# Kernel optimization log

Measured on AMD Instinct MI355X. Metric: run time of the kernel, lower is better.

The kernel has to match this reference:

```python
import jax, jax.numpy as jnp
import numpy as np

N_HEADS = 16


def setup_inputs() -> dict:
    key = jax.random.key(0)
    k_x, k_q, k_k, k_v, k_o = jax.random.split(key, 5)
    N, S, D = 8, 4096, 1024
    scale = 0.02
    return {
        "x": jax.random.normal(k_x, (N, S, D), dtype=jnp.float32),
        "Wq": jax.random.normal(k_q, (D, D), dtype=jnp.float32) * scale,
        "Wk": jax.random.normal(k_k, (D, D), dtype=jnp.float32) * scale,
        "Wv": jax.random.normal(k_v, (D, D), dtype=jnp.float32) * scale,
        "Wo": jax.random.normal(k_o, (D, D), dtype=jnp.float32) * scale,
        "bo": jnp.zeros((D,), dtype=jnp.float32),
    }


def reference(x, Wq, Wk, Wv, Wo, bo):
    N, S, D = x.shape
    H = N_HEADS
    hd = D // H
    # torch nn.Linear: y = x @ W.T (no bias for q/k/v)
    q = (x @ Wq.T).reshape(N, S, H, hd).transpose(0, 2, 1, 3)  # (N, H, S, hd)
    k = (x @ Wk.T).reshape(N, S, H, hd).transpose(0, 2, 1, 3)
    v = (x @ Wv.T).reshape(N, S, H, hd).transpose(0, 2, 1, 3)
    # Faithful to source: labels q/k bind to the HEADS axis of the permuted
    # tensors, h binds to the sequence axis -> attention over heads, shape
    # (N, S, H, H).
    att = jnp.einsum('nqhd,nkhd->nhqk', q, k)
    att = jax.nn.softmax(att / jnp.sqrt(jnp.asarray(hd, x.dtype)), axis=3)
    out = jnp.einsum('nhqk,nkhd->nqhd', att, v).reshape(N, S, D)
    return out @ Wo.T + bo
```

## Files before the change

kernel.cpp:

```cpp
#include <hip/hip_runtime.h>
#include <hip/hip_bf16.h>
#include <stdint.h>

typedef __hip_bfloat16 bf16;
typedef __attribute__((ext_vector_type(8))) short short8;
typedef __attribute__((ext_vector_type(4))) float f32x4;

__device__ __forceinline__ unsigned short f2bf(float f) {
    bf16 h = __float2bfloat16(f);
    union { bf16 h; unsigned short u; } c; c.h = h; return c.u;
}
__device__ __forceinline__ unsigned int pack2(float a, float b) {
    return (unsigned int)f2bf(a) | ((unsigned int)f2bf(b) << 16);
}

__device__ __forceinline__ void gld16(const void* g, void* l) {
    __builtin_amdgcn_global_load_lds(
        (const __attribute__((address_space(1))) void*)g,
        (__attribute__((address_space(3))) void*)l, 16, 0, 0);
}

__global__ __launch_bounds__(256) void cvt_f32_bf16(
    const float* __restrict__ in, unsigned short* __restrict__ out, long n4)
{
    long i = (long)blockIdx.x * 256 + threadIdx.x;
    if (i >= n4) return;
    float4 v = ((const float4*)in)[i];
    ushort4 o;
    o.x = f2bf(v.x); o.y = f2bf(v.y); o.z = f2bf(v.z); o.w = f2bf(v.w);
    ((ushort4*)out)[i] = o;
}

__global__ __launch_bounds__(256) void cvt_w4(
    const float* __restrict__ a, const float* __restrict__ b,
    const float* __restrict__ c, const float* __restrict__ d,
    unsigned short* __restrict__ out)
{
    const float* src = (blockIdx.y == 0) ? a : (blockIdx.y == 1) ? b
                     : (blockIdx.y == 2) ? c : d;
    long i = (long)blockIdx.x * 256 + threadIdx.x;
    float4 v = ((const float4*)src)[i];
    ushort4 o;
    o.x = f2bf(v.x); o.y = f2bf(v.y); o.z = f2bf(v.z); o.w = f2bf(v.w);
    ((ushort4*)(out + (size_t)blockIdx.y * 1048576))[i] = o;
}

#define BM 128
#define BN 128
#define BK 32

__device__ __forceinline__ void store_c(bf16* C, size_t idx, float v) {
    C[idx] = __float2bfloat16(v);
}
__device__ __forceinline__ void store_c(float* C, size_t idx, float v) {
    C[idx] = v;
}

template <typename CT>
__device__ __forceinline__ void gemm_body(
    const bf16* __restrict__ A, const bf16* __restrict__ B,
    CT* __restrict__ C, const float* __restrict__ bias,
    int M, int N, int K)
{
    __shared__ char smem[(BM * BK + BN * BK) * 2];
    char* sA = smem;
    char* sB = smem + BM * BK * 2;

    const int t    = threadIdx.x;
    const int lane = t & 63;
    const int wave = t >> 6;
    const int wm   = wave & 1;
    const int wn   = wave >> 1;
    const int l16  = lane & 15;
    const int quad = lane >> 4;

    const int rowBase = blockIdx.y * BM;
    const int colBase = blockIdx.x * BN;

    f32x4 acc[4][4];
#pragma unroll
    for (int i = 0; i < 4; i++)
#pragma unroll
        for (int j = 0; j < 4; j++) acc[i][j] = (f32x4){0.f, 0.f, 0.f, 0.f};

    const int c1 = t, c2 = t + 256;
    const int r1 = c1 >> 2, o1 = (c1 & 3) * 8;
    const int r2 = c2 >> 2, o2 = (c2 & 3) * 8;

    for (int k0 = 0; k0 < K; k0 += BK) {
        __syncthreads();
        gld16(A + (size_t)(rowBase + r1) * K + k0 + o1, sA + c1 * 16);
        gld16(A + (size_t)(rowBase + r2) * K + k0 + o2, sA + c2 * 16);
        gld16(B + (size_t)(colBase + r1) * K + k0 + o1, sB + c1 * 16);
        gld16(B + (size_t)(colBase + r2) * K + k0 + o2, sB + c2 * 16);
        __syncthreads();

        short8 af[4], bf[4];
#pragma unroll
        for (int mt = 0; mt < 4; mt++)
            af[mt] = *(const short8*)(sA + (wm * 64 + mt * 16 + l16) * 64 + quad * 16);
#pragma unroll
        for (int nt = 0; nt < 4; nt++)
            bf[nt] = *(const short8*)(sB + (wn * 64 + nt * 16 + l16) * 64 + quad * 16);

#pragma unroll
        for (int mt = 0; mt < 4; mt++)
#pragma unroll
            for (int nt = 0; nt < 4; nt++)
                acc[mt][nt] = __builtin_amdgcn_mfma_f32_16x16x32_bf16(
                    af[mt], bf[nt], acc[mt][nt], 0, 0, 0);
    }

#pragma unroll
    for (int nt = 0; nt < 4; nt++) {
        int col = colBase + wn * 64 + nt * 16 + l16;
        float bv = bias ? bias[col] : 0.f;
#pragma unroll
        for (int mt = 0; mt < 4; mt++) {
            int row0 = rowBase + wm * 64 + mt * 16 + quad * 4;
#pragma unroll
            for (int r = 0; r < 4; r++) {
                store_c(C, (size_t)(row0 + r) * N + col, acc[mt][nt][r] + bv);
            }
        }
    }
}

__global__ __launch_bounds__(256) void gemm_qkv(
    const bf16* __restrict__ A, const bf16* __restrict__ B,
    bf16* __restrict__ C, int M, int N, int K)
{
    gemm_body<bf16>(A, B, C, nullptr, M, N, K);
}

__global__ __launch_bounds__(256) void gemm_proj(
    const bf16* __restrict__ A, const bf16* __restrict__ B,
    float* __restrict__ C, const float* __restrict__ bias,
    int M, int N, int K)
{
    gemm_body<float>(A, B, C, bias, M, N, K);
}

__global__ __launch_bounds__(256) void attn_heads(
    const bf16* __restrict__ QKV, bf16* __restrict__ Y)
{
    __shared__ char smem[4 * 3264];
    const int t    = threadIdx.x;
    const int lane = t & 63;
    const int wave = t >> 6;
    const int l16  = lane & 15;
    const int quad = lane >> 4;

    char* Vp = smem + wave * 3264;
    char* Pp = smem + wave * 3264 + 2240;

    const long pos = (long)blockIdx.x * 4 + wave;
    const int  n   = (int)(pos >> 12);
    const int  s   = (int)(pos & 4095);
    const bf16* base = QKV + pos * 3072;

    uint4 v0 = *(const uint4*)(base + 2048 + lane * 8);
    uint4 v1 = *(const uint4*)(base + 2560 + lane * 8);
    short8 qa0 = *(const short8*)(base +        l16 * 64 + quad * 8);
    short8 qa1 = *(const short8*)(base +        l16 * 64 + quad * 8 + 32);
    short8 kb0 = *(const short8*)(base + 1024 + l16 * 64 + quad * 8);
    short8 kb1 = *(const short8*)(base + 1024 + l16 * 64 + quad * 8 + 32);

    {
        int kh0 = lane >> 3, c = lane & 7;
        *(uint4*)(Vp + kh0 * 136 + c * 16) = v0;
        *(uint4*)(Vp + (kh0 + 8) * 136 + c * 16) = v1;
    }

    *(f32x4*)(Pp + lane * 16) = (f32x4){0.f, 0.f, 0.f, 0.f};

    f32x4 sacc = (f32x4){0.f, 0.f, 0.f, 0.f};
    sacc = __builtin_amdgcn_mfma_f32_16x16x32_bf16(qa0, kb0, sacc, 0, 0, 0);
    sacc = __builtin_amdgcn_mfma_f32_16x16x32_bf16(qa1, kb1, sacc, 0, 0, 0);

    float e[4], sm[4];
#pragma unroll
    for (int r = 0; r < 4; r++) { e[r] = __expf(sacc[r] * 0.125f); sm[r] = e[r]; }
#pragma unroll
    for (int m = 1; m <= 8; m <<= 1) {
#pragma unroll
        for (int r = 0; r < 4; r++) sm[r] += __shfl_xor(sm[r], m);
    }
#pragma unroll
    for (int r = 0; r < 4; r++) {
        float p = e[r] * __builtin_amdgcn_rcpf(sm[r]);
        *(unsigned short*)(Pp + (quad * 4 + r) * 64 + l16 * 2) = f2bf(p);
    }

    short8 pfrag = *(const short8*)(Pp + l16 * 64 + quad * 16);

    const char* gbase = Vp + (quad & 1) * (8 * 136)
                           + ((l16 >> 3) * 16) + ((l16 & 7) * 2);
    const size_t yb = ((size_t)n * 4096 + (size_t)(s >> 4)) * 1024
                    + (size_t)(s & 15) * 64;
#pragma unroll
    for (int f = 0; f < 4; f++) {
        short8 vfrag;
#pragma unroll
        for (int j = 0; j < 8; j++)
            vfrag[j] = *(const short*)(gbase + f * 32 + j * 136);
        f32x4 oc = __builtin_amdgcn_mfma_f32_16x16x32_bf16(
            vfrag, pfrag, (f32x4){0.f, 0.f, 0.f, 0.f}, 0, 0, 0);
        uint2 w;
        w.x = pack2(oc[0], oc[1]);
        w.y = pack2(oc[2], oc[3]);
        *(uint2*)(Y + yb + (size_t)l16 * 262144 + 16 * f + quad * 4) = w;
    }
}

extern "C" void kernel_launch(void* const* d_in, const int* in_sizes, int n_in,
                              void* d_out, int out_size, void* d_ws, size_t ws_size,
                              hipStream_t stream) {
    const float* x  = (const float*)d_in[0];
    const float* Wq = (const float*)d_in[1];
    const float* Wk = (const float*)d_in[2];
    const float* Wv = (const float*)d_in[3];
    const float* Wo = (const float*)d_in[4];
    const float* bo = (const float*)d_in[5];
    float* out = (float*)d_out;

    const int M = 8 * 4096;
    const size_t MN = (size_t)M * 1024;

    bf16* Qkv  = (bf16*)d_ws;
    bf16* Xb   = Qkv + (size_t)M * 3072;
    bf16* Yb   = Xb;
    bf16* Wcat = Xb + MN;
    bf16* Wob  = Wcat + (size_t)3072 * 1024;

    {
        long n4 = (long)MN / 4;
        cvt_f32_bf16<<<dim3((unsigned)(n4 / 256)), dim3(256), 0, stream>>>(
            x, (unsigned short*)Xb, n4);
        cvt_w4<<<dim3(1024, 4), dim3(256), 0, stream>>>(
            Wq, Wk, Wv, Wo, (unsigned short*)Wcat);
    }

    dim3 block(256);
    gemm_qkv<<<dim3(3072 / BN, M / BM), block, 0, stream>>>(
        Xb, Wcat, Qkv, M, 3072, 1024);
    attn_heads<<<dim3(M / 4), block, 0, stream>>>(Qkv, Yb);
    gemm_proj<<<dim3(1024 / BN, M / BM), block, 0, stream>>>(
        Yb, Wob, out, bo, M, 1024, 1024);
}
```

Measured before the change: 650.2 us.

## Rewrite GEMMs as 256x256 tiles with double-buffered swizzled LDS pipeline

```diff
diff --git a/kernel.cpp b/kernel.cpp
--- a/kernel.cpp
+++ b/kernel.cpp
@@ -45,9 +45,6 @@
     ((ushort4*)(out + (size_t)blockIdx.y * 1048576))[i] = o;
 }
 
-#define BM 128
-#define BN 128
-#define BK 32
 
 __device__ __forceinline__ void store_c(bf16* C, size_t idx, float v) {
     C[idx] = __float2bfloat16(v);
@@ -57,88 +54,152 @@
 }
 
 template <typename CT>
-__device__ __forceinline__ void gemm_body(
+__device__ __forceinline__ void gemm_body256(
     const bf16* __restrict__ A, const bf16* __restrict__ B,
     CT* __restrict__ C, const float* __restrict__ bias,
     int M, int N, int K)
 {
-    __shared__ char smem[(BM * BK + BN * BK) * 2];
-    char* sA = smem;
-    char* sB = smem + BM * BK * 2;
+    __shared__ char smem[131072];
 
     const int t    = threadIdx.x;
     const int lane = t & 63;
     const int wave = t >> 6;
-    const int wm   = wave & 1;
-    const int wn   = wave >> 1;
+    const int wm   = wave >> 2;
+    const int wn   = wave & 3;
     const int l16  = lane & 15;
     const int quad = lane >> 4;
 
-    const int rowBase = blockIdx.y * BM;
-    const int colBase = blockIdx.x * BN;
-
-    f32x4 acc[4][4];
-#pragma unroll
-    for (int i = 0; i < 4; i++)
-#pragma unroll
-        for (int j = 0; j < 4; j++) acc[i][j] = (f32x4){0.f, 0.f, 0.f, 0.f};
-
-    const int c1 = t, c2 = t + 256;
-    const int r1 = c1 >> 2, o1 = (c1 & 3) * 8;
-    const int r2 = c2 >> 2, o2 = (c2 & 3) * 8;
-
-    for (int k0 = 0; k0 < K; k0 += BK) {
-        __syncthreads();
-        gld16(A + (size_t)(rowBase + r1) * K + k0 + o1, sA + c1 * 16);
-        gld16(A + (size_t)(rowBase + r2) * K + k0 + o2, sA + c2 * 16);
-        gld16(B + (size_t)(colBase + r1) * K + k0 + o1, sB + c1 * 16);
-        gld16(B + (size_t)(colBase + r2) * K + k0 + o2, sB + c2 * 16);
-        __syncthreads();
-
-        short8 af[4], bf[4];
-#pragma unroll
-        for (int mt = 0; mt < 4; mt++)
-            af[mt] = *(const short8*)(sA + (wm * 64 + mt * 16 + l16) * 64 + quad * 16);
-#pragma unroll
-        for (int nt = 0; nt < 4; nt++)
-            bf[nt] = *(const short8*)(sB + (wn * 64 + nt * 16 + l16) * 64 + quad * 16);
-
-#pragma unroll
-        for (int mt = 0; mt < 4; mt++)
-#pragma unroll
-            for (int nt = 0; nt < 4; nt++)
-                acc[mt][nt] = __builtin_amdgcn_mfma_f32_16x16x32_bf16(
-                    af[mt], bf[nt], acc[mt][nt], 0, 0, 0);
-    }
-
-#pragma unroll
-    for (int nt = 0; nt < 4; nt++) {
-        int col = colBase + wn * 64 + nt * 16 + l16;
+    const int gy   = M >> 8;
+    const int nwg  = (N >> 8) * gy;
+    const int orig = blockIdx.x;
+    const int wg   = (orig & 7) * (nwg >> 3) + (orig >> 3);
+    const int bx   = wg / gy;
+    const int by   = wg - bx * gy;
+
+    const int rowBase = by << 8;
+    const int colBase = bx << 8;
+
+    size_t offA[4], offB[4];
+    int ldsOff[4];
+#pragma unroll
+    for (int r = 0; r < 4; ++r) {
+        int i   = (r << 9) + t;
+        int row = i >> 3;
+        int sw  = ((i & 7) << 4) ^ ((row & 7) << 4);
+        offA[r] = (size_t)(rowBase + row) * K + (sw >> 1);
+        offB[r] = (size_t)(colBase + row) * K + (sw >> 1);
+        ldsOff[r] = i << 4;
+    }
+
+    auto stage = [&](int bufsel, int k0) {
+        char* bA_ = smem + (bufsel << 16);
+        char* bB_ = bA_ + 32768;
+#pragma unroll
+        for (int r = 0; r < 4; ++r) {
+            gld16(A + offA[r] + k0, bA_ + ldsOff[r]);
+            gld16(B + offB[r] + k0, bB_ + ldsOff[r]);
+        }
+    };
+
+    f32x4 acc[8][4];
+#pragma unroll
+    for (int i = 0; i < 8; ++i)
+#pragma unroll
+        for (int j = 0; j < 4; ++j) acc[i][j] = (f32x4){0.f, 0.f, 0.f, 0.f};
+
+    const int xr   = (l16 & 7) << 4;
+    const int kq0  = ((quad << 4)) ^ xr;
+    const int kq1  = (64 + (quad << 4)) ^ xr;
+    const int aRowB = ((wm << 7) + l16) << 7;
+    const int bRowB = ((wn << 6) + l16) << 7;
+
+    stage(0, 0);
+    stage(1, 64);
+    asm volatile("s_waitcnt vmcnt(8)" ::: "memory");
+    __builtin_amdgcn_s_barrier();
+
+    const int ntiles = K >> 6;
+    int cur = 0;
+    for (int tt = 0; tt < ntiles; ++tt) {
+        char* sA = smem + (cur << 16);
+        char* sB = sA + 32768;
+
+        short8 a0[8], b0[4];
+#pragma unroll
+        for (int mt = 0; mt < 8; ++mt)
+            a0[mt] = *(const short8*)(sA + aRowB + mt * 2048 + kq0);
+#pragma unroll
+        for (int nt2 = 0; nt2 < 4; ++nt2)
+            b0[nt2] = *(const short8*)(sB + bRowB + nt2 * 2048 + kq0);
+
+        __builtin_amdgcn_s_setprio(1);
+#pragma unroll
+        for (int mt = 0; mt < 8; ++mt)
+#pragma unroll
+            for (int nt2 = 0; nt2 < 4; ++nt2)
+                acc[mt][nt2] = __builtin_amdgcn_mfma_f32_16x16x32_bf16(
+                    a0[mt], b0[nt2], acc[mt][nt2], 0, 0, 0);
+        __builtin_amdgcn_s_setprio(0);
+
+        short8 a1[8], b1[4];
+#pragma unroll
+        for (int mt = 0; mt < 8; ++mt)
+            a1[mt] = *(const short8*)(sA + aRowB + mt * 2048 + kq1);
+#pragma unroll
+        for (int nt2 = 0; nt2 < 4; ++nt2)
+            b1[nt2] = *(const short8*)(sB + bRowB + nt2 * 2048 + kq1);
+
+        asm volatile("s_waitcnt lgkmcnt(0)" ::: "memory");
+        __builtin_amdgcn_s_barrier();
+
+        if (tt + 2 < ntiles) stage(cur, (tt + 2) << 6);
+
+        __builtin_amdgcn_s_setprio(1);
+#pragma unroll
+        for (int mt = 0; mt < 8; ++mt)
+#pragma unroll
+            for (int nt2 = 0; nt2 < 4; ++nt2)
+                acc[mt][nt2] = __builtin_amdgcn_mfma_f32_16x16x32_bf16(
+                    a1[mt], b1[nt2], acc[mt][nt2], 0, 0, 0);
+        __builtin_amdgcn_s_setprio(0);
+
+        if (tt + 1 < ntiles) {
+            if (tt + 2 < ntiles)
+                asm volatile("s_waitcnt vmcnt(8)" ::: "memory");
+            else
+                asm volatile("s_waitcnt vmcnt(0)" ::: "memory");
+            __builtin_amdgcn_s_barrier();
+        }
+        cur ^= 1;
+    }
+
+#pragma unroll
+    for (int nt2 = 0; nt2 < 4; ++nt2) {
+        int col = colBase + (wn << 6) + (nt2 << 4) + l16;
         float bv = bias ? bias[col] : 0.f;
 #pragma unroll
-        for (int mt = 0; mt < 4; mt++) {
-            int row0 = rowBase + wm * 64 + mt * 16 + quad * 4;
-#pragma unroll
-            for (int r = 0; r < 4; r++) {
-                store_c(C, (size_t)(row0 + r) * N + col, acc[mt][nt][r] + bv);
-            }
+        for (int mt = 0; mt < 8; ++mt) {
+            int row0 = rowBase + (wm << 7) + (mt << 4) + (quad << 2);
+#pragma unroll
+            for (int r = 0; r < 4; ++r)
+                store_c(C, (size_t)(row0 + r) * N + col, acc[mt][nt2][r] + bv);
         }
     }
 }
 
-__global__ __launch_bounds__(256) void gemm_qkv(
+__global__ __launch_bounds__(512, 2) void gemm_qkv(
     const bf16* __restrict__ A, const bf16* __restrict__ B,
     bf16* __restrict__ C, int M, int N, int K)
 {
-    gemm_body<bf16>(A, B, C, nullptr, M, N, K);
-}
-
-__global__ __launch_bounds__(256) void gemm_proj(
+    gemm_body256<bf16>(A, B, C, nullptr, M, N, K);
+}
+
+__global__ __launch_bounds__(512, 2) void gemm_proj(
     const bf16* __restrict__ A, const bf16* __restrict__ B,
     float* __restrict__ C, const float* __restrict__ bias,
     int M, int N, int K)
 {
-    gemm_body<float>(A, B, C, bias, M, N, K);
+    gemm_body256<float>(A, B, C, bias, M, N, K);
 }
 
 __global__ __launch_bounds__(256) void attn_heads(
@@ -241,10 +302,10 @@
             Wq, Wk, Wv, Wo, (unsigned short*)Wcat);
     }
 
-    dim3 block(256);
-    gemm_qkv<<<dim3(3072 / BN, M / BM), block, 0, stream>>>(
+    dim3 block(512);
+    gemm_qkv<<<dim3((3072 / 256) * (M / 256)), block, 0, stream>>>(
         Xb, Wcat, Qkv, M, 3072, 1024);
-    attn_heads<<<dim3(M / 4), block, 0, stream>>>(Qkv, Yb);
-    gemm_proj<<<dim3(1024 / BN, M / BM), block, 0, stream>>>(
+    attn_heads<<<dim3(M / 4), dim3(256), 0, stream>>>(Qkv, Yb);
+    gemm_proj<<<dim3((1024 / 256) * (M / 256)), block, 0, stream>>>(
         Yb, Wob, out, bo, M, 1024, 1024);
 }
```

Result: faster. 592.4 us (-8.9%).
